# Kernel tuning notes

Measured on AMD Instinct MI355X. Metric: run time of the kernel, lower is better.

## Reference

```python
import jax, jax.numpy as jnp
import numpy as np

N = 50000
D = 64
E = 800000


def setup_inputs() -> dict:
    key = jax.random.key(0)
    ks = jax.random.split(key, 8)
    x = jax.random.normal(ks[0], (N, D), dtype=jnp.float32)
    edge_index = jax.random.randint(ks[1], (2, E), 0, N, dtype=jnp.int64)
    edge_attr = jax.random.normal(ks[2], (E,), dtype=jnp.float32)
    x_agg_emb = jax.random.normal(ks[3], (N, D), dtype=jnp.float32)
    # Linear(2D -> D) weights stored as [in, out]; scale ~ kaiming-ish
    W_msg = jax.random.normal(ks[4], (2 * D, D), dtype=jnp.float32) * (1.0 / np.sqrt(2 * D))
    b_msg = jnp.zeros((D,), dtype=jnp.float32)
    W_upd = jax.random.normal(ks[5], (2 * D, D), dtype=jnp.float32) * (1.0 / np.sqrt(2 * D))
    b_upd = jnp.zeros((D,), dtype=jnp.float32)
    return {"x": x, "edge_index": edge_index, "edge_attr": edge_attr,
            "x_agg_emb": x_agg_emb, "W_msg": W_msg, "b_msg": b_msg,
            "W_upd": W_upd, "b_upd": b_upd}


def reference(x, edge_index, edge_attr, x_agg_emb, W_msg, b_msg, W_upd, b_upd):
    col, row = edge_index[0], edge_index[1]
    # edge-weighted gather: [E, D]
    msgs = edge_attr[:, None] * x[col]
    # scatter-mean over destination nodes (dim_size = N)
    summed = jax.ops.segment_sum(msgs, row, num_segments=N)            # [N, D]
    counts = jax.ops.segment_sum(jnp.ones_like(edge_attr), row, num_segments=N)  # [N]
    x_agg = summed / jnp.maximum(counts, 1.0)[:, None]
    # message MLP: Linear(2D->D) + ReLU
    m = jax.nn.relu(jnp.concatenate([x_agg, x_agg_emb], axis=-1) @ W_msg + b_msg)
    # update MLP: Linear(2D->D) + ReLU
    out = jax.nn.relu(jnp.concatenate([x, m], axis=-1) @ W_upd + b_upd)
    return out
```

## Files before the change

### kernel.cpp

```cpp
#include <hip/hip_runtime.h>


#define CAP 48
#define FILLB 2048
#define CVTB 1024

typedef __attribute__((ext_vector_type(8))) short short8;
typedef __attribute__((ext_vector_type(4))) float f32x4;

__device__ __forceinline__ unsigned short f2bf(float f) {
    unsigned int u = __float_as_uint(f);
    u += 0x7FFFu + ((u >> 16) & 1u);
    return (unsigned short)(u >> 16);
}
__device__ __forceinline__ float bf2f(unsigned short h) {
    return __uint_as_float((unsigned)h << 16);
}
__device__ __forceinline__ uint4 pack8(const float* v) {
    uint4 r;
    r.x = (unsigned)f2bf(v[0]) | ((unsigned)f2bf(v[1]) << 16);
    r.y = (unsigned)f2bf(v[2]) | ((unsigned)f2bf(v[3]) << 16);
    r.z = (unsigned)f2bf(v[4]) | ((unsigned)f2bf(v[5]) << 16);
    r.w = (unsigned)f2bf(v[6]) | ((unsigned)f2bf(v[7]) << 16);
    return r;
}

__global__ __launch_bounds__(256) void zero_f32(float* p, int n) {
    int i = blockIdx.x * 256 + threadIdx.x;
    if (i < n) p[i] = 0.0f;
}
__global__ __launch_bounds__(256) void zero_i32(int* p, int n) {
    int i = blockIdx.x * 256 + threadIdx.x;
    if (i < n) p[i] = 0;
}

__global__ __launch_bounds__(256) void cvt_zero_group(
    const float* __restrict__ x, unsigned short* __restrict__ xh,
    int* __restrict__ cnt, uint4* __restrict__ pk4, int N)
{
    const int g    = blockIdx.x & 7;
    const int bg   = blockIdx.x >> 3;
    const int nb   = gridDim.x >> 3;
    const int rpg  = (N + 7) >> 3;
    const int rlo  = g * rpg;
    const int rhi  = min(rlo + rpg, N);
    const int nrows = rhi - rlo;
    const int tid  = bg * 256 + (int)threadIdx.x;
    const int nthr = nb * 256;

    for (int c = tid; c < nrows * 8; c += nthr) {
        size_t base = ((size_t)rlo * 8 + c) * 8;
        const float* src = x + base;
        float4 p0 = ((const float4*)src)[0];
        float4 p1 = ((const float4*)src)[1];
        float v[8];
        v[0] = p0.x; v[1] = p0.y; v[2] = p0.z; v[3] = p0.w;
        v[4] = p1.x; v[5] = p1.y; v[6] = p1.z; v[7] = p1.w;
        *(uint4*)&xh[base] = pack8(v);
    }
    for (int c = tid; c < nrows; c += nthr) cnt[rlo + c] = 0;
    const uint4 z = make_uint4(0u, 0u, 0u, 0u);
    const size_t pbase = (size_t)rlo * (CAP / 2);
    for (size_t c = tid; c < (size_t)nrows * (CAP / 2); c += nthr)
        pk4[pbase + c] = z;
}

__global__ __launch_bounds__(256) void fill_group_kernel(
    const int* __restrict__ ei, const float* __restrict__ ea,
    int* cnt, int2* __restrict__ packed, int E, int N)
{
    const int g   = blockIdx.x & 7;
    const int bg  = blockIdx.x >> 3;
    const int nb  = gridDim.x >> 3;
    const int rpg = (N + 7) >> 3;
    const int rlo = g * rpg;
    const int rhi = min(rlo + rpg, N);
    const int chunk = (E + nb - 1) / nb;
    const int lo = bg * chunk;
    const int hi = min(lo + chunk, E);
    int e = lo + (int)threadIdx.x;
    for (; e + 768 < hi; e += 1024) {
        int r0 = ei[E + e];
        int r1 = ei[E + e + 256];
        int r2 = ei[E + e + 512];
        int r3 = ei[E + e + 768];
        int c0 = ei[e], c1 = ei[e + 256], c2 = ei[e + 512], c3 = ei[e + 768];
        float a0 = ea[e], a1 = ea[e + 256], a2 = ea[e + 512], a3 = ea[e + 768];
        bool m0 = (r0 >= rlo) & (r0 < rhi);
        bool m1 = (r1 >= rlo) & (r1 < rhi);
        bool m2 = (r2 >= rlo) & (r2 < rhi);
        bool m3 = (r3 >= rlo) & (r3 < rhi);
        int p0 = CAP, p1 = CAP, p2 = CAP, p3 = CAP;
        if (m0) p0 = atomicAdd(&cnt[r0], 1);
        if (m1) p1 = atomicAdd(&cnt[r1], 1);
        if (m2) p2 = atomicAdd(&cnt[r2], 1);
        if (m3) p3 = atomicAdd(&cnt[r3], 1);
        if (m0 && p0 < CAP) packed[(size_t)r0 * CAP + p0] = make_int2(c0, __float_as_int(a0));
        if (m1 && p1 < CAP) packed[(size_t)r1 * CAP + p1] = make_int2(c1, __float_as_int(a1));
        if (m2 && p2 < CAP) packed[(size_t)r2 * CAP + p2] = make_int2(c2, __float_as_int(a2));
        if (m3 && p3 < CAP) packed[(size_t)r3 * CAP + p3] = make_int2(c3, __float_as_int(a3));
    }
    for (; e < hi; e += 256) {
        int row = ei[E + e];
        if (row >= rlo && row < rhi) {
            int pos = atomicAdd(&cnt[row], 1);
            if (pos < CAP)
                packed[(size_t)row * CAP + pos] = make_int2(ei[e], __float_as_int(ea[e]));
        }
    }
}


__device__ __forceinline__ void stage_W512(
    unsigned short* Wb, const float* Wg, int t)
{
    #pragma unroll
    for (int c = t; c < 1024; c += 512) {
        int R = c >> 6, nn = c & 63;
        int kt = R >> 2, qq = R & 3;
        const float* src = Wg + (size_t)(kt * 32 + qq * 8) * 64 + nn;
        float v[8];
        #pragma unroll
        for (int j = 0; j < 8; j++) v[j] = src[(size_t)j * 64];
        *(uint4*)&Wb[R * 528 + nn * 8] = pack8(v);
    }
}

__global__ __launch_bounds__(512, 6) void gather_mlp(
    const int2* __restrict__ packed, const int* __restrict__ cnt,
    const unsigned short* __restrict__ xh, const float* __restrict__ emb,
    const float* __restrict__ Wm, const float* __restrict__ bm,
    const float* __restrict__ Wu, const float* __restrict__ bu,
    float* __restrict__ out, int N)
{
    __shared__ __align__(16) unsigned short Ab [64 * 128];
    __shared__ __align__(16) unsigned short Wb [16 * 528];
    __shared__ __align__(16) unsigned short Wb2[16 * 528];

    const int t    = threadIdx.x;
    const int g    = blockIdx.x & 7;
    const int tile = blockIdx.x >> 3;
    const int rpg  = (N + 7) >> 3;
    const int rlo  = g * rpg;
    const int rhi  = min(rlo + rpg, N);
    const int tile0 = rlo + tile * 64;
    const int lane = t & 63;
    const int q = lane >> 4, ln = lane & 15;
    const unsigned lane2 = (unsigned)lane * 2;
    const int wu = __builtin_amdgcn_readfirstlane(t >> 6);

    stage_W512(Wb,  Wm, t);
    stage_W512(Wb2, Wu, t);
    const int sr = t >> 3, sc = t & 7;
    uint4 xreg = make_uint4(0u, 0u, 0u, 0u);
    if (tile0 + sr < rhi)
        xreg = *(const uint4*)&xh[(size_t)(tile0 + sr) * 64 + sc * 8];
    {
        int node = tile0 + sr;
        float v[8] = {0.f, 0.f, 0.f, 0.f, 0.f, 0.f, 0.f, 0.f};
        if (node < rhi) {
            const float* src = emb + (size_t)node * 64 + sc * 8;
            float4 p0 = ((const float4*)src)[0];
            float4 p1 = ((const float4*)src)[1];
            v[0] = p0.x; v[1] = p0.y; v[2] = p0.z; v[3] = p0.w;
            v[4] = p1.x; v[5] = p1.y; v[6] = p1.z; v[7] = p1.w;
        }
        int ch = 8 + sc;
        *(uint4*)&Ab[sr * 128 + ((ch ^ (sr & 15)) * 8)] = pack8(v);
    }

    const int4* sp[8];
    int deg[8];
    int maxdl = 0;
    #pragma unroll
    for (int n = 0; n < 8; n++) {
        int node = tile0 + wu * 8 + n;
        bool ok = node < rhi;
        int nd = ok ? node : rlo;
        sp[n] = (const int4*)packed + (size_t)nd * (CAP / 2);
        deg[n] = ok ? __builtin_amdgcn_readfirstlane(cnt[node]) : 0;
        maxdl = max(maxdl, min(deg[n], CAP));
    }
    float ac0[8], ac1[8];
    #pragma unroll
    for (int n = 0; n < 8; n++) { ac0[n] = 0.f; ac1[n] = 0.f; }

    const int maxb = (maxdl + 1) >> 1;
    for (int jb = 0; jb < maxb; jb++) {
        {
            int4 d0 = sp[0][jb], d1 = sp[1][jb], d2 = sp[2][jb], d3 = sp[3][jb];
            unsigned short u00 = *(const unsigned short*)((const char*)xh + (((unsigned)d0.x << 7) + lane2));
            unsigned short u01 = *(const unsigned short*)((const char*)xh + (((unsigned)d0.z << 7) + lane2));
            unsigned short u10 = *(const unsigned short*)((const char*)xh + (((unsigned)d1.x << 7) + lane2));
            unsigned short u11 = *(const unsigned short*)((const char*)xh + (((unsigned)d1.z << 7) + lane2));
            unsigned short u20 = *(const unsigned short*)((const char*)xh + (((unsigned)d2.x << 7) + lane2));
            unsigned short u21 = *(const unsigned short*)((const char*)xh + (((unsigned)d2.z << 7) + lane2));
            unsigned short u30 = *(const unsigned short*)((const char*)xh + (((unsigned)d3.x << 7) + lane2));
            unsigned short u31 = *(const unsigned short*)((const char*)xh + (((unsigned)d3.z << 7) + lane2));
            ac0[0] += __int_as_float(d0.y) * bf2f(u00);
            ac1[0] += __int_as_float(d0.w) * bf2f(u01);
            ac0[1] += __int_as_float(d1.y) * bf2f(u10);
            ac1[1] += __int_as_float(d1.w) * bf2f(u11);
            ac0[2] += __int_as_float(d2.y) * bf2f(u20);
            ac1[2] += __int_as_float(d2.w) * bf2f(u21);
            ac0[3] += __int_as_float(d3.y) * bf2f(u30);
            ac1[3] += __int_as_float(d3.w) * bf2f(u31);
        }
        {
            int4 d0 = sp[4][jb], d1 = sp[5][jb], d2 = sp[6][jb], d3 = sp[7][jb];
            unsigned short u00 = *(const unsigned short*)((const char*)xh + (((unsigned)d0.x << 7) + lane2));
            unsigned short u01 = *(const unsigned short*)((const char*)xh + (((unsigned)d0.z << 7) + lane2));
            unsigned short u10 = *(const unsigned short*)((const char*)xh + (((unsigned)d1.x << 7) + lane2));
            unsigned short u11 = *(const unsigned short*)((const char*)xh + (((unsigned)d1.z << 7) + lane2));
            unsigned short u20 = *(const unsigned short*)((const char*)xh + (((unsigned)d2.x << 7) + lane2));
            unsigned short u21 = *(const unsigned short*)((const char*)xh + (((unsigned)d2.z << 7) + lane2));
            unsigned short u30 = *(const unsigned short*)((const char*)xh + (((unsigned)d3.x << 7) + lane2));
            unsigned short u31 = *(const unsigned short*)((const char*)xh + (((unsigned)d3.z << 7) + lane2));
            ac0[4] += __int_as_float(d0.y) * bf2f(u00);
            ac1[4] += __int_as_float(d0.w) * bf2f(u01);
            ac0[5] += __int_as_float(d1.y) * bf2f(u10);
            ac1[5] += __int_as_float(d1.w) * bf2f(u11);
            ac0[6] += __int_as_float(d2.y) * bf2f(u20);
            ac1[6] += __int_as_float(d2.w) * bf2f(u21);
            ac0[7] += __int_as_float(d3.y) * bf2f(u30);
            ac1[7] += __int_as_float(d3.w) * bf2f(u31);
        }
    }

    #pragma unroll
    for (int n = 0; n < 8; n++) {
        int r = wu * 8 + n;
        int node = tile0 + r;
        float mean = (node < rhi)
            ? (ac0[n] + ac1[n]) / fmaxf((float)deg[n], 1.0f) : 0.f;
        int ch = lane >> 3;
        Ab[r * 128 + ((ch ^ (r & 15)) * 8) + (lane & 7)] = f2bf(mean);
    }
    __syncthreads();

    const int wr = wu & 3;
    const int wn0 = (wu >> 2) * 2, wn1 = wn0 + 1;
    f32x4 acc0 = (f32x4){0.f, 0.f, 0.f, 0.f};
    f32x4 acc1 = (f32x4){0.f, 0.f, 0.f, 0.f};
    {
        const int rr = wr * 16 + ln;
        #pragma unroll
        for (int kt = 0; kt < 4; kt++) {
            short8 af = *(const short8*)&Ab[rr * 128 + (((kt * 4 + q) ^ ln) * 8)];
            short8 bf0 = *(const short8*)&Wb[(kt * 4 + q) * 528 + (wn0 * 16 + ln) * 8];
            short8 bf1 = *(const short8*)&Wb[(kt * 4 + q) * 528 + (wn1 * 16 + ln) * 8];
            acc0 = __builtin_amdgcn_mfma_f32_16x16x32_bf16(af, bf0, acc0, 0, 0, 0);
            acc1 = __builtin_amdgcn_mfma_f32_16x16x32_bf16(af, bf1, acc1, 0, 0, 0);
        }
    }
    __syncthreads();

    *(uint4*)&Ab[sr * 128 + ((sc ^ (sr & 15)) * 8)] = xreg;
    {
        float bmv0 = bm[wn0 * 16 + ln];
        float bmv1 = bm[wn1 * 16 + ln];
        #pragma unroll
        for (int reg = 0; reg < 4; reg++) {
            int rr = wr * 16 + q * 4 + reg;
            {
                float mv = fmaxf(acc0[reg] + bmv0, 0.f);
                int k  = 64 + wn0 * 16 + ln;
                int ch = k >> 3;
                Ab[rr * 128 + ((ch ^ (rr & 15)) * 8) + (k & 7)] = f2bf(mv);
            }
            {
                float mv = fmaxf(acc1[reg] + bmv1, 0.f);
                int k  = 64 + wn1 * 16 + ln;
                int ch = k >> 3;
                Ab[rr * 128 + ((ch ^ (rr & 15)) * 8) + (k & 7)] = f2bf(mv);
            }
        }
    }
    __syncthreads();

    f32x4 acc2a = (f32x4){0.f, 0.f, 0.f, 0.f};
    f32x4 acc2b = (f32x4){0.f, 0.f, 0.f, 0.f};
    {
        const int rr = wr * 16 + ln;
        #pragma unroll
        for (int kt = 0; kt < 4; kt++) {
            short8 af = *(const short8*)&Ab[rr * 128 + (((kt * 4 + q) ^ ln) * 8)];
            short8 bf0 = *(const short8*)&Wb2[(kt * 4 + q) * 528 + (wn0 * 16 + ln) * 8];
            short8 bf1 = *(const short8*)&Wb2[(kt * 4 + q) * 528 + (wn1 * 16 + ln) * 8];
            acc2a = __builtin_amdgcn_mfma_f32_16x16x32_bf16(af, bf0, acc2a, 0, 0, 0);
            acc2b = __builtin_amdgcn_mfma_f32_16x16x32_bf16(af, bf1, acc2b, 0, 0, 0);
        }
    }
    {
        float buv0 = bu[wn0 * 16 + ln];
        float buv1 = bu[wn1 * 16 + ln];
        #pragma unroll
        for (int reg = 0; reg < 4; reg++) {
            int rr = wr * 16 + q * 4 + reg;
            int node = tile0 + rr;
            if (node < rhi) {
                out[(size_t)node * 64 + wn0 * 16 + ln] = fmaxf(acc2a[reg] + buv0, 0.f);
                out[(size_t)node * 64 + wn1 * 16 + ln] = fmaxf(acc2b[reg] + buv1, 0.f);
            }
        }
    }
}


__global__ __launch_bounds__(256) void hist_kernel(
    const int* __restrict__ ei, int* hist, int E)
{
    int e = blockIdx.x * 256 + threadIdx.x;
    if (e < E) atomicAdd(&hist[ei[E + e]], 1);
}
__global__ __launch_bounds__(256) void scan_partial_kernel(
    const int* __restrict__ hist, int* partial, int N)
{
    __shared__ int s[256];
    int t = threadIdx.x;
    int i = blockIdx.x * 256 + t;
    s[t] = (i < N) ? hist[i] : 0;
    __syncthreads();
    #pragma unroll
    for (int off = 128; off > 0; off >>= 1) {
        if (t < off) s[t] += s[t + off];
        __syncthreads();
    }
    if (t == 0) partial[blockIdx.x] = s[0];
}
__global__ __launch_bounds__(256) void scan_top_kernel(
    const int* __restrict__ partial, int* scanP, int NB)
{
    __shared__ int s[256];
    int t = threadIdx.x;
    int v = (t < NB) ? partial[t] : 0;
    s[t] = v;
    __syncthreads();
    #pragma unroll
    for (int off = 1; off < 256; off <<= 1) {
        int add = (t >= off) ? s[t - off] : 0;
        __syncthreads();
        s[t] += add;
        __syncthreads();
    }
    if (t < NB) scanP[t] = s[t] - v;
}
__global__ __launch_bounds__(256) void scan_final_kernel(
    const int* __restrict__ hist, const int* __restrict__ scanP,
    int* offsets, int* cursor, int N)
{
    __shared__ int s[256];
    int t = threadIdx.x;
    int i = blockIdx.x * 256 + t;
    int v = (i < N) ? hist[i] : 0;
    s[t] = v;
    __syncthreads();
    #pragma unroll
    for (int off = 1; off < 256; off <<= 1) {
        int add = (t >= off) ? s[t - off] : 0;
        __syncthreads();
        s[t] += add;
        __syncthreads();
    }
    if (i < N) {
        int o = scanP[blockIdx.x] + s[t] - v;
        offsets[i] = o;
        cursor[i]  = o;
    }
}
__global__ __launch_bounds__(256) void fill_kernel(
    const int* __restrict__ ei, const float* __restrict__ ea,
    int* cursor, int2* __restrict__ packed, int E)
{
    int e = blockIdx.x * 256 + threadIdx.x;
    if (e >= E) return;
    int pos = atomicAdd(&cursor[ei[E + e]], 1);
    packed[pos] = make_int2(ei[e], __float_as_int(ea[e]));
}
__global__ __launch_bounds__(256) void gather_kernel(
    const int2* __restrict__ packed, const int* __restrict__ offsets,
    const int* __restrict__ hist, const float* __restrict__ x,
    float* __restrict__ out, int N)
{
    int t = threadIdx.x;
    int n = blockIdx.x * 4 + (t >> 6);
    int lane = t & 63;
    if (n >= N) return;
    int start = offsets[n];
    int deg   = hist[n];
    float a0 = 0.f, a1 = 0.f, a2 = 0.f, a3 = 0.f;
    int j = 0;
    for (; j + 4 <= deg; j += 4) {
        int2 p0 = packed[start + j];
        int2 p1 = packed[start + j + 1];
        int2 p2 = packed[start + j + 2];
        int2 p3 = packed[start + j + 3];
        a0 += __int_as_float(p0.y) * x[(size_t)p0.x * 64 + lane];
        a1 += __int_as_float(p1.y) * x[(size_t)p1.x * 64 + lane];
        a2 += __int_as_float(p2.y) * x[(size_t)p2.x * 64 + lane];
        a3 += __int_as_float(p3.y) * x[(size_t)p3.x * 64 + lane];
    }
    for (; j < deg; j++) {
        int2 p = packed[start + j];
        a0 += __int_as_float(p.y) * x[(size_t)p.x * 64 + lane];
    }
    float acc = (a0 + a1) + (a2 + a3);
    out[(size_t)n * 64 + lane] = acc / fmaxf((float)deg, 1.0f);
}


__global__ __launch_bounds__(256) void scatter_kernel(
    const int* __restrict__ ei, const float* __restrict__ ea,
    const float* __restrict__ x, float* summed, float* counts, int E)
{
    int idx = blockIdx.x * 256 + threadIdx.x;
    int e = idx >> 6;
    int d = idx & 63;
    if (e >= E) return;
    float v = ea[e] * x[(size_t)ei[e] * 64 + d];
    atomicAdd(&summed[(size_t)ei[E + e] * 64 + d], v);
    if (d == 0) atomicAdd(&counts[ei[E + e]], 1.0f);
}


__device__ __forceinline__ void stage_W(
    unsigned short* Wb, const float* Wg, int t)
{
    #pragma unroll
    for (int c = t; c < 1024; c += 256) {
        int R = c >> 6, nn = c & 63;
        int kt = R >> 2, qq = R & 3;
        const float* src = Wg + (size_t)(kt * 32 + qq * 8) * 64 + nn;
        float v[8];
        #pragma unroll
        for (int j = 0; j < 8; j++) v[j] = src[(size_t)j * 64];
        *(uint4*)&Wb[R * 528 + nn * 8] = pack8(v);
    }
}

__device__ __forceinline__ void mfma_tile(
    const unsigned short* Ab, const unsigned short* Wb,
    int wv, int lane, f32x4 acc[4])
{
    const int q  = lane >> 4;
    const int ln = lane & 15;
    const int rr = wv * 16 + ln;
    short8 af[4];
    #pragma unroll
    for (int kt = 0; kt < 4; kt++)
        af[kt] = *(const short8*)&Ab[rr * 128 + (((kt * 4 + q) ^ ln) * 8)];
    #pragma unroll
    for (int nt = 0; nt < 4; nt++) {
        #pragma unroll
        for (int kt = 0; kt < 4; kt++) {
            short8 bf = *(const short8*)&Wb[(kt * 4 + q) * 528 + (nt * 16 + ln) * 8];
            acc[nt] = __builtin_amdgcn_mfma_f32_16x16x32_bf16(af[kt], bf, acc[nt], 0, 0, 0);
        }
    }
}

__global__ __launch_bounds__(256) void mfma_mlp(
    const float* Aagg, const float* __restrict__ Aemb,
    const float* __restrict__ counts, const float* __restrict__ Xin,
    const float* __restrict__ Wm, const float* __restrict__ bm,
    const float* __restrict__ Wu, const float* __restrict__ bu,
    float* out, int N)
{
    __shared__ __align__(16) unsigned short Ab[64 * 128];
    __shared__ __align__(16) unsigned short Wb[16 * 528];

    const int t = threadIdx.x;
    const int tile0 = blockIdx.x * 64;
    const int lane = t & 63, wv = t >> 6;
    const int q = lane >> 4, ln = lane & 15;

    stage_W(Wb, Wm, t);
    #pragma unroll
    for (int s = t; s < 1024; s += 256) {
        int r = s >> 4, chunk = s & 15;
        int node = tile0 + r;
        float v[8] = {0.f, 0.f, 0.f, 0.f, 0.f, 0.f, 0.f, 0.f};
        if (node < N) {
            const float* src = (chunk < 8)
                ? (Aagg + (size_t)node * 64 + chunk * 8)
                : (Aemb + (size_t)node * 64 + (chunk - 8) * 8);
            float4 p0 = ((const float4*)src)[0];
            float4 p1 = ((const float4*)src)[1];
            v[0] = p0.x; v[1] = p0.y; v[2] = p0.z; v[3] = p0.w;
            v[4] = p1.x; v[5] = p1.y; v[6] = p1.z; v[7] = p1.w;
            if (counts && chunk < 8) {
                float rc = 1.0f / fmaxf(counts[node], 1.0f);
                #pragma unroll
                for (int i = 0; i < 8; i++) v[i] *= rc;
            }
        }
        *(uint4*)&Ab[r * 128 + ((chunk ^ (r & 15)) * 8)] = pack8(v);
    }
    __syncthreads();

    f32x4 acc[4];
    #pragma unroll
    for (int nt = 0; nt < 4; nt++) acc[nt] = (f32x4){0.f, 0.f, 0.f, 0.f};
    mfma_tile(Ab, Wb, wv, lane, acc);
    __syncthreads();

    stage_W(Wb, Wu, t);
    #pragma unroll
    for (int s = t; s < 512; s += 256) {
        int r = s >> 3, chunk = s & 7;
        int node = tile0 + r;
        float v[8] = {0.f, 0.f, 0.f, 0.f, 0.f, 0.f, 0.f, 0.f};
        if (node < N) {
            const float* src = Xin + (size_t)node * 64 + chunk * 8;
            float4 p0 = ((const float4*)src)[0];
            float4 p1 = ((const float4*)src)[1];
            v[0] = p0.x; v[1] = p0.y; v[2] = p0.z; v[3] = p0.w;
            v[4] = p1.x; v[5] = p1.y; v[6] = p1.z; v[7] = p1.w;
        }
        *(uint4*)&Ab[r * 128 + ((chunk ^ (r & 15)) * 8)] = pack8(v);
    }
    #pragma unroll
    for (int nt = 0; nt < 4; nt++) {
        float bmv = bm[nt * 16 + ln];
        #pragma unroll
        for (int reg = 0; reg < 4; reg++) {
            float mv = fmaxf(acc[nt][reg] + bmv, 0.f);
            int rr = wv * 16 + q * 4 + reg;
            int k  = 64 + nt * 16 + ln;
            int ch = k >> 3;
            Ab[rr * 128 + ((ch ^ (rr & 15)) * 8) + (k & 7)] = f2bf(mv);
        }
    }
    __syncthreads();

    f32x4 acc2[4];
    #pragma unroll
    for (int nt = 0; nt < 4; nt++) acc2[nt] = (f32x4){0.f, 0.f, 0.f, 0.f};
    mfma_tile(Ab, Wb, wv, lane, acc2);
    #pragma unroll
    for (int nt = 0; nt < 4; nt++) {
        float buv = bu[nt * 16 + ln];
        #pragma unroll
        for (int reg = 0; reg < 4; reg++) {
            int rr = wv * 16 + q * 4 + reg;
            int node = tile0 + rr;
            if (node < N)
                out[(size_t)node * 64 + nt * 16 + ln] =
                    fmaxf(acc2[nt][reg] + buv, 0.f);
        }
    }
}

extern "C" void kernel_launch(void* const* d_in, const int* in_sizes, int n_in,
                              void* d_out, int out_size, void* d_ws, size_t ws_size,
                              hipStream_t stream) {
    const float* x   = (const float*)d_in[0];
    const int*   ei  = (const int*)d_in[1];
    const float* ea  = (const float*)d_in[2];
    const float* emb = (const float*)d_in[3];
    const float* Wm  = (const float*)d_in[4];
    const float* bm  = (const float*)d_in[5];
    const float* Wu  = (const float*)d_in[6];
    const float* bu  = (const float*)d_in[7];
    float*       out = (float*)d_out;

    const int N = in_sizes[0] / 64;
    const int E = in_sizes[2];
    const int NB = (N + 255) / 256;

    const int eblocks = (E + 255) / 256;
    const int mblocks = (N + 63) / 64;
    const int rpg = (N + 7) / 8;

    const size_t need_cap = (size_t)N * CAP * 8 + (size_t)N * 128 + (size_t)N * 4;
    const size_t need_csr = (size_t)E * 8 + ((size_t)3 * N + 512) * 4;

    if (ws_size >= need_cap) {
        char* ws = (char*)d_ws;
        int2*           packed = (int2*)ws;
        unsigned short* xh     = (unsigned short*)(ws + (size_t)N * CAP * 8);
        int*            cnt    = (int*)(ws + (size_t)N * CAP * 8 + (size_t)N * 128);

        cvt_zero_group<<<CVTB, 256, 0, stream>>>(x, xh, cnt, (uint4*)packed, N);
        fill_group_kernel<<<FILLB, 256, 0, stream>>>(ei, ea, cnt, packed, E, N);
        int tpg = (rpg + 63) / 64;
        gather_mlp<<<8 * tpg, 512, 0, stream>>>(packed, cnt, xh, emb,
                                                Wm, bm, Wu, bu, out, N);
    } else if (ws_size >= need_csr && NB <= 256) {
        char* ws = (char*)d_ws;
        int2* packed  = (int2*)ws;
        int*  hist    = (int*)(ws + (size_t)E * 8);
        int*  offsets = hist + N;
        int*  cursor  = offsets + N;
        int*  partial = cursor + N;
        int*  scanP   = partial + 256;

        zero_i32<<<NB, 256, 0, stream>>>(hist, N);
        hist_kernel<<<eblocks, 256, 0, stream>>>(ei, hist, E);
        scan_partial_kernel<<<NB, 256, 0, stream>>>(hist, partial, N);
        scan_top_kernel<<<1, 256, 0, stream>>>(partial, scanP, NB);
        scan_final_kernel<<<NB, 256, 0, stream>>>(hist, scanP, offsets, cursor, N);
        fill_kernel<<<eblocks, 256, 0, stream>>>(ei, ea, cursor, packed, E);
        gather_kernel<<<(N + 3) / 4, 256, 0, stream>>>(packed, offsets, hist, x, out, N);
        mfma_mlp<<<mblocks, 256, 0, stream>>>(out, emb, nullptr, x,
                                              Wm, bm, Wu, bu, out, N);
    } else {
        float* counts = (float*)d_ws;
        zero_f32<<<(N * 64 + 255) / 256, 256, 0, stream>>>(out, N * 64);
        zero_f32<<<NB, 256, 0, stream>>>(counts, N);
        long long total = (long long)E * 64;
        scatter_kernel<<<(int)((total + 255) / 256), 256, 0, stream>>>(
            ei, ea, x, out, counts, E);
        mfma_mlp<<<mblocks, 256, 0, stream>>>(out, emb, counts, x,
                                              Wm, bm, Wu, bu, out, N);
    }
}
```

Measured before the change: 163.8 us.

## Fuse convert, fill and gather-MLP into one cooperative kernel with grid syncs

Replaces the three-kernel sequence (convert/zero, bucketed fill, gather+MLP) with a single cooperative kernel of 512 blocks that separates the phases with grid-wide syncs and loops over tiles persistently. The aim is to remove the launch gaps and tail effects between kernels. The cost is two grid barriers, a fixed grid size that may underfill or overfill the device, and a lower occupancy hint. The fallback gather_mlp also drops readfirstlane on the degrees and loses its occupancy hint.

After: 506.5 us. +209.1%, slower.

```diff
diff --git a/kernel.cpp b/kernel.cpp
--- a/kernel.cpp
+++ b/kernel.cpp
@@ -1,7 +1,11 @@
 #include <hip/hip_runtime.h>
+#include <hip/hip_cooperative_groups.h>
+
+namespace cg = cooperative_groups;
 
 
 #define CAP 48
+#define FGRID 512
 #define FILLB 2048
 #define CVTB 1024
 
@@ -33,6 +37,275 @@
     int i = blockIdx.x * 256 + threadIdx.x;
     if (i < n) p[i] = 0;
 }
+
+__device__ __forceinline__ void stage_W512(
+    unsigned short* Wb, const float* Wg, int t)
+{
+    #pragma unroll
+    for (int c = t; c < 1024; c += 512) {
+        int R = c >> 6, nn = c & 63;
+        int kt = R >> 2, qq = R & 3;
+        const float* src = Wg + (size_t)(kt * 32 + qq * 8) * 64 + nn;
+        float v[8];
+        #pragma unroll
+        for (int j = 0; j < 8; j++) v[j] = src[(size_t)j * 64];
+        *(uint4*)&Wb[R * 528 + nn * 8] = pack8(v);
+    }
+}
+
+__global__ __launch_bounds__(512, 4) void fused_all(
+    const float* __restrict__ x, const int* __restrict__ ei,
+    const float* __restrict__ ea, const float* __restrict__ emb,
+    const float* __restrict__ Wm, const float* __restrict__ bm,
+    const float* __restrict__ Wu, const float* __restrict__ bu,
+    float* __restrict__ out, int2* __restrict__ packed,
+    unsigned short* __restrict__ xh, int* __restrict__ cnt,
+    int N, int E)
+{
+    __shared__ __align__(16) unsigned short Ab [64 * 128];
+    __shared__ __align__(16) unsigned short Wb [16 * 528];
+    __shared__ __align__(16) unsigned short Wb2[16 * 528];
+
+    cg::grid_group grid = cg::this_grid();
+
+    const int t   = threadIdx.x;
+    const int g   = blockIdx.x & 7;
+    const int bg  = blockIdx.x >> 3;
+    const int nb  = gridDim.x >> 3;
+    const int rpg = (N + 7) >> 3;
+    const int rlo = g * rpg;
+    const int rhi = min(rlo + rpg, N);
+    const int nrows = rhi - rlo;
+
+    {
+        const int tid  = bg * 512 + t;
+        const int nthr = nb * 512;
+        for (int c = tid; c < nrows * 8; c += nthr) {
+            size_t base = ((size_t)rlo * 8 + c) * 8;
+            const float* src = x + base;
+            float4 p0 = ((const float4*)src)[0];
+            float4 p1 = ((const float4*)src)[1];
+            float v[8];
+            v[0] = p0.x; v[1] = p0.y; v[2] = p0.z; v[3] = p0.w;
+            v[4] = p1.x; v[5] = p1.y; v[6] = p1.z; v[7] = p1.w;
+            *(uint4*)&xh[base] = pack8(v);
+        }
+        for (int c = tid; c < nrows; c += nthr) cnt[rlo + c] = 0;
+        const uint4 z = make_uint4(0u, 0u, 0u, 0u);
+        uint4* pk4 = (uint4*)packed;
+        const size_t pbase = (size_t)rlo * (CAP / 2);
+        for (int c = tid; c < nrows * (CAP / 2); c += nthr)
+            pk4[pbase + c] = z;
+    }
+    __threadfence();
+    grid.sync();
+
+    {
+        const int chunk = (E + nb - 1) / nb;
+        const int lo = bg * chunk;
+        const int hi = min(lo + chunk, E);
+        int e = lo + t;
+        for (; e + 1536 < hi; e += 2048) {
+            int r0 = ei[E + e], r1 = ei[E + e + 512];
+            int r2 = ei[E + e + 1024], r3 = ei[E + e + 1536];
+            int c0 = ei[e], c1 = ei[e + 512], c2 = ei[e + 1024], c3 = ei[e + 1536];
+            float a0 = ea[e], a1 = ea[e + 512], a2 = ea[e + 1024], a3 = ea[e + 1536];
+            bool m0 = (r0 >= rlo) & (r0 < rhi);
+            bool m1 = (r1 >= rlo) & (r1 < rhi);
+            bool m2 = (r2 >= rlo) & (r2 < rhi);
+            bool m3 = (r3 >= rlo) & (r3 < rhi);
+            int p0 = CAP, p1 = CAP, p2 = CAP, p3 = CAP;
+            if (m0) p0 = atomicAdd(&cnt[r0], 1);
+            if (m1) p1 = atomicAdd(&cnt[r1], 1);
+            if (m2) p2 = atomicAdd(&cnt[r2], 1);
+            if (m3) p3 = atomicAdd(&cnt[r3], 1);
+            if (m0 && p0 < CAP) packed[(size_t)r0 * CAP + p0] = make_int2(c0, __float_as_int(a0));
+            if (m1 && p1 < CAP) packed[(size_t)r1 * CAP + p1] = make_int2(c1, __float_as_int(a1));
+            if (m2 && p2 < CAP) packed[(size_t)r2 * CAP + p2] = make_int2(c2, __float_as_int(a2));
+            if (m3 && p3 < CAP) packed[(size_t)r3 * CAP + p3] = make_int2(c3, __float_as_int(a3));
+        }
+        for (; e < hi; e += 512) {
+            int row = ei[E + e];
+            if (row >= rlo && row < rhi) {
+                int pos = atomicAdd(&cnt[row], 1);
+                if (pos < CAP)
+                    packed[(size_t)row * CAP + pos] = make_int2(ei[e], __float_as_int(ea[e]));
+            }
+        }
+    }
+    __threadfence();
+    grid.sync();
+
+    stage_W512(Wb,  Wm, t);
+    stage_W512(Wb2, Wu, t);
+
+    const int lane = t & 63;
+    const int q = lane >> 4, ln = lane & 15;
+    const unsigned lane2 = (unsigned)lane * 2;
+    const int wu = __builtin_amdgcn_readfirstlane(t >> 6);
+    const int wr = wu & 3;
+    const int wn0 = (wu >> 2) * 2, wn1 = wn0 + 1;
+    const int sr = t >> 3, sc = t & 7;
+    const int TPG = (rpg + 63) >> 6;
+
+    for (int tile = bg; tile < TPG; tile += nb) {
+        const int tile0 = rlo + tile * 64;
+
+        uint4 xreg = make_uint4(0u, 0u, 0u, 0u);
+        if (tile0 + sr < rhi)
+            xreg = *(const uint4*)&xh[(size_t)(tile0 + sr) * 64 + sc * 8];
+        {
+            int node = tile0 + sr;
+            float v[8] = {0.f, 0.f, 0.f, 0.f, 0.f, 0.f, 0.f, 0.f};
+            if (node < rhi) {
+                const float* src = emb + (size_t)node * 64 + sc * 8;
+                float4 p0 = ((const float4*)src)[0];
+                float4 p1 = ((const float4*)src)[1];
+                v[0] = p0.x; v[1] = p0.y; v[2] = p0.z; v[3] = p0.w;
+                v[4] = p1.x; v[5] = p1.y; v[6] = p1.z; v[7] = p1.w;
+            }
+            int ch = 8 + sc;
+            *(uint4*)&Ab[sr * 128 + ((ch ^ (sr & 15)) * 8)] = pack8(v);
+        }
+
+        int seg[8], deg[8];
+        int maxdl = 0;
+        #pragma unroll
+        for (int n = 0; n < 8; n++) {
+            int node = tile0 + wu * 8 + n;
+            bool ok = node < rhi;
+            seg[n] = (ok ? node : rlo) * (CAP / 2);
+            deg[n] = ok ? cnt[node] : 0;
+            maxdl = max(maxdl, min(deg[n], CAP));
+        }
+        float ac0[8], ac1[8];
+        #pragma unroll
+        for (int n = 0; n < 8; n++) { ac0[n] = 0.f; ac1[n] = 0.f; }
+
+        const int4* s4 = (const int4*)packed;
+        const int maxb = (maxdl + 1) >> 1;
+        for (int jb = 0; jb < maxb; jb++) {
+            {
+                int4 d0 = s4[seg[0] + jb], d1 = s4[seg[1] + jb];
+                int4 d2 = s4[seg[2] + jb], d3 = s4[seg[3] + jb];
+                unsigned short u00 = *(const unsigned short*)((const char*)xh + (((unsigned)d0.x << 7) + lane2));
+                unsigned short u01 = *(const unsigned short*)((const char*)xh + (((unsigned)d0.z << 7) + lane2));
+                unsigned short u10 = *(const unsigned short*)((const char*)xh + (((unsigned)d1.x << 7) + lane2));
+                unsigned short u11 = *(const unsigned short*)((const char*)xh + (((unsigned)d1.z << 7) + lane2));
+                unsigned short u20 = *(const unsigned short*)((const char*)xh + (((unsigned)d2.x << 7) + lane2));
+                unsigned short u21 = *(const unsigned short*)((const char*)xh + (((unsigned)d2.z << 7) + lane2));
+                unsigned short u30 = *(const unsigned short*)((const char*)xh + (((unsigned)d3.x << 7) + lane2));
+                unsigned short u31 = *(const unsigned short*)((const char*)xh + (((unsigned)d3.z << 7) + lane2));
+                ac0[0] += __int_as_float(d0.y) * bf2f(u00);
+                ac1[0] += __int_as_float(d0.w) * bf2f(u01);
+                ac0[1] += __int_as_float(d1.y) * bf2f(u10);
+                ac1[1] += __int_as_float(d1.w) * bf2f(u11);
+                ac0[2] += __int_as_float(d2.y) * bf2f(u20);
+                ac1[2] += __int_as_float(d2.w) * bf2f(u21);
+                ac0[3] += __int_as_float(d3.y) * bf2f(u30);
+                ac1[3] += __int_as_float(d3.w) * bf2f(u31);
+            }
+            {
+                int4 d0 = s4[seg[4] + jb], d1 = s4[seg[5] + jb];
+                int4 d2 = s4[seg[6] + jb], d3 = s4[seg[7] + jb];
+                unsigned short u00 = *(const unsigned short*)((const char*)xh + (((unsigned)d0.x << 7) + lane2));
+                unsigned short u01 = *(const unsigned short*)((const char*)xh + (((unsigned)d0.z << 7) + lane2));
+                unsigned short u10 = *(const unsigned short*)((const char*)xh + (((unsigned)d1.x << 7) + lane2));
+                unsigned short u11 = *(const unsigned short*)((const char*)xh + (((unsigned)d1.z << 7) + lane2));
+                unsigned short u20 = *(const unsigned short*)((const char*)xh + (((unsigned)d2.x << 7) + lane2));
+                unsigned short u21 = *(const unsigned short*)((const char*)xh + (((unsigned)d2.z << 7) + lane2));
+                unsigned short u30 = *(const unsigned short*)((const char*)xh + (((unsigned)d3.x << 7) + lane2));
+                unsigned short u31 = *(const unsigned short*)((const char*)xh + (((unsigned)d3.z << 7) + lane2));
+                ac0[4] += __int_as_float(d0.y) * bf2f(u00);
+                ac1[4] += __int_as_float(d0.w) * bf2f(u01);
+                ac0[5] += __int_as_float(d1.y) * bf2f(u10);
+                ac1[5] += __int_as_float(d1.w) * bf2f(u11);
+                ac0[6] += __int_as_float(d2.y) * bf2f(u20);
+                ac1[6] += __int_as_float(d2.w) * bf2f(u21);
+                ac0[7] += __int_as_float(d3.y) * bf2f(u30);
+                ac1[7] += __int_as_float(d3.w) * bf2f(u31);
+            }
+        }
+
+        #pragma unroll
+        for (int n = 0; n < 8; n++) {
+            int r = wu * 8 + n;
+            int node = tile0 + r;
+            float mean = (node < rhi)
+                ? (ac0[n] + ac1[n]) / fmaxf((float)deg[n], 1.0f) : 0.f;
+            int ch = lane >> 3;
+            Ab[r * 128 + ((ch ^ (r & 15)) * 8) + (lane & 7)] = f2bf(mean);
+        }
+        __syncthreads();
+
+        f32x4 acc0 = (f32x4){0.f, 0.f, 0.f, 0.f};
+        f32x4 acc1 = (f32x4){0.f, 0.f, 0.f, 0.f};
+        {
+            const int rr = wr * 16 + ln;
+            #pragma unroll
+            for (int kt = 0; kt < 4; kt++) {
+                short8 af  = *(const short8*)&Ab[rr * 128 + (((kt * 4 + q) ^ ln) * 8)];
+                short8 bf0 = *(const short8*)&Wb[(kt * 4 + q) * 528 + (wn0 * 16 + ln) * 8];
+                short8 bf1 = *(const short8*)&Wb[(kt * 4 + q) * 528 + (wn1 * 16 + ln) * 8];
+                acc0 = __builtin_amdgcn_mfma_f32_16x16x32_bf16(af, bf0, acc0, 0, 0, 0);
+                acc1 = __builtin_amdgcn_mfma_f32_16x16x32_bf16(af, bf1, acc1, 0, 0, 0);
+            }
+        }
+        __syncthreads();
+
+        *(uint4*)&Ab[sr * 128 + ((sc ^ (sr & 15)) * 8)] = xreg;
+        {
+            float bmv0 = bm[wn0 * 16 + ln];
+            float bmv1 = bm[wn1 * 16 + ln];
+            #pragma unroll
+            for (int reg = 0; reg < 4; reg++) {
+                int rr = wr * 16 + q * 4 + reg;
+                {
+                    float mv = fmaxf(acc0[reg] + bmv0, 0.f);
+                    int k  = 64 + wn0 * 16 + ln;
+                    int ch = k >> 3;
+                    Ab[rr * 128 + ((ch ^ (rr & 15)) * 8) + (k & 7)] = f2bf(mv);
+                }
+                {
+                    float mv = fmaxf(acc1[reg] + bmv1, 0.f);
+                    int k  = 64 + wn1 * 16 + ln;
+                    int ch = k >> 3;
+                    Ab[rr * 128 + ((ch ^ (rr & 15)) * 8) + (k & 7)] = f2bf(mv);
+                }
+            }
+        }
+        __syncthreads();
+
+        f32x4 acc2a = (f32x4){0.f, 0.f, 0.f, 0.f};
+        f32x4 acc2b = (f32x4){0.f, 0.f, 0.f, 0.f};
+        {
+            const int rr = wr * 16 + ln;
+            #pragma unroll
+            for (int kt = 0; kt < 4; kt++) {
+                short8 af  = *(const short8*)&Ab[rr * 128 + (((kt * 4 + q) ^ ln) * 8)];
+                short8 bf0 = *(const short8*)&Wb2[(kt * 4 + q) * 528 + (wn0 * 16 + ln) * 8];
+                short8 bf1 = *(const short8*)&Wb2[(kt * 4 + q) * 528 + (wn1 * 16 + ln) * 8];
+                acc2a = __builtin_amdgcn_mfma_f32_16x16x32_bf16(af, bf0, acc2a, 0, 0, 0);
+                acc2b = __builtin_amdgcn_mfma_f32_16x16x32_bf16(af, bf1, acc2b, 0, 0, 0);
+            }
+        }
+        {
+            float buv0 = bu[wn0 * 16 + ln];
+            float buv1 = bu[wn1 * 16 + ln];
+            #pragma unroll
+            for (int reg = 0; reg < 4; reg++) {
+                int rr = wr * 16 + q * 4 + reg;
+                int node = tile0 + rr;
+                if (node < rhi) {
+                    out[(size_t)node * 64 + wn0 * 16 + ln] = fmaxf(acc2a[reg] + buv0, 0.f);
+                    out[(size_t)node * 64 + wn1 * 16 + ln] = fmaxf(acc2b[reg] + buv1, 0.f);
+                }
+            }
+        }
+        __syncthreads();
+    }
+}
+
 
 __global__ __launch_bounds__(256) void cvt_zero_group(
     const float* __restrict__ x, unsigned short* __restrict__ xh,
@@ -110,23 +383,7 @@
     }
 }
 
-
-__device__ __forceinline__ void stage_W512(
-    unsigned short* Wb, const float* Wg, int t)
-{
-    #pragma unroll
-    for (int c = t; c < 1024; c += 512) {
-        int R = c >> 6, nn = c & 63;
-        int kt = R >> 2, qq = R & 3;
-        const float* src = Wg + (size_t)(kt * 32 + qq * 8) * 64 + nn;
-        float v[8];
-        #pragma unroll
-        for (int j = 0; j < 8; j++) v[j] = src[(size_t)j * 64];
-        *(uint4*)&Wb[R * 528 + nn * 8] = pack8(v);
-    }
-}
-
-__global__ __launch_bounds__(512, 6) void gather_mlp(
+__global__ __launch_bounds__(512) void gather_mlp(
     const int2* __restrict__ packed, const int* __restrict__ cnt,
     const unsigned short* __restrict__ xh, const float* __restrict__ emb,
     const float* __restrict__ Wm, const float* __restrict__ bm,
@@ -169,26 +426,28 @@
         *(uint4*)&Ab[sr * 128 + ((ch ^ (sr & 15)) * 8)] = pack8(v);
     }
 
-    const int4* sp[8];
-    int deg[8];
+    int seg[8], deg[8];
     int maxdl = 0;
     #pragma unroll
     for (int n = 0; n < 8; n++) {
         int node = tile0 + wu * 8 + n;
         bool ok = node < rhi;
-        int nd = ok ? node : rlo;
-        sp[n] = (const int4*)packed + (size_t)nd * (CAP / 2);
-        deg[n] = ok ? __builtin_amdgcn_readfirstlane(cnt[node]) : 0;
+        seg[n] = (ok ? node : rlo) * (CAP / 2);
+        deg[n] = ok ? cnt[node] : 0;
         maxdl = max(maxdl, min(deg[n], CAP));
     }
     float ac0[8], ac1[8];
     #pragma unroll
     for (int n = 0; n < 8; n++) { ac0[n] = 0.f; ac1[n] = 0.f; }
 
+    const int4* s4 = (const int4*)packed;
     const int maxb = (maxdl + 1) >> 1;
     for (int jb = 0; jb < maxb; jb++) {
-        {
-            int4 d0 = sp[0][jb], d1 = sp[1][jb], d2 = sp[2][jb], d3 = sp[3][jb];
+        #pragma unroll
+        for (int h = 0; h < 2; h++) {
+            int b = h * 4;
+            int4 d0 = s4[seg[b] + jb], d1 = s4[seg[b + 1] + jb];
+            int4 d2 = s4[seg[b + 2] + jb], d3 = s4[seg[b + 3] + jb];
             unsigned short u00 = *(const unsigned short*)((const char*)xh + (((unsigned)d0.x << 7) + lane2));
             unsigned short u01 = *(const unsigned short*)((const char*)xh + (((unsigned)d0.z << 7) + lane2));
             unsigned short u10 = *(const unsigned short*)((const char*)xh + (((unsigned)d1.x << 7) + lane2));
@@ -197,33 +456,14 @@
             unsigned short u21 = *(const unsigned short*)((const char*)xh + (((unsigned)d2.z << 7) + lane2));
             unsigned short u30 = *(const unsigned short*)((const char*)xh + (((unsigned)d3.x << 7) + lane2));
             unsigned short u31 = *(const unsigned short*)((const char*)xh + (((unsigned)d3.z << 7) + lane2));
-            ac0[0] += __int_as_float(d0.y) * bf2f(u00);
-            ac1[0] += __int_as_float(d0.w) * bf2f(u01);
-            ac0[1] += __int_as_float(d1.y) * bf2f(u10);
-            ac1[1] += __int_as_float(d1.w) * bf2f(u11);
-            ac0[2] += __int_as_float(d2.y) * bf2f(u20);
-            ac1[2] += __int_as_float(d2.w) * bf2f(u21);
-            ac0[3] += __int_as_float(d3.y) * bf2f(u30);
-            ac1[3] += __int_as_float(d3.w) * bf2f(u31);
-        }
-        {
-            int4 d0 = sp[4][jb], d1 = sp[5][jb], d2 = sp[6][jb], d3 = sp[7][jb];
-            unsigned short u00 = *(const unsigned short*)((const char*)xh + (((unsigned)d0.x << 7) + lane2));
-            unsigned short u01 = *(const unsigned short*)((const char*)xh + (((unsigned)d0.z << 7) + lane2));
-            unsigned short u10 = *(const unsigned short*)((const char*)xh + (((unsigned)d1.x << 7) + lane2));
-            unsigned short u11 = *(const unsigned short*)((const char*)xh + (((unsigned)d1.z << 7) + lane2));
-            unsigned short u20 = *(const unsigned short*)((const char*)xh + (((unsigned)d2.x << 7) + lane2));
-            unsigned short u21 = *(const unsigned short*)((const char*)xh + (((unsigned)d2.z << 7) + lane2));
-            unsigned short u30 = *(const unsigned short*)((const char*)xh + (((unsigned)d3.x << 7) + lane2));
-            unsigned short u31 = *(const unsigned short*)((const char*)xh + (((unsigned)d3.z << 7) + lane2));
-            ac0[4] += __int_as_float(d0.y) * bf2f(u00);
-            ac1[4] += __int_as_float(d0.w) * bf2f(u01);
-            ac0[5] += __int_as_float(d1.y) * bf2f(u10);
-            ac1[5] += __int_as_float(d1.w) * bf2f(u11);
-            ac0[6] += __int_as_float(d2.y) * bf2f(u20);
-            ac1[6] += __int_as_float(d2.w) * bf2f(u21);
-            ac0[7] += __int_as_float(d3.y) * bf2f(u30);
-            ac1[7] += __int_as_float(d3.w) * bf2f(u31);
+            ac0[b]     += __int_as_float(d0.y) * bf2f(u00);
+            ac1[b]     += __int_as_float(d0.w) * bf2f(u01);
+            ac0[b + 1] += __int_as_float(d1.y) * bf2f(u10);
+            ac1[b + 1] += __int_as_float(d1.w) * bf2f(u11);
+            ac0[b + 2] += __int_as_float(d2.y) * bf2f(u20);
+            ac1[b + 2] += __int_as_float(d2.w) * bf2f(u21);
+            ac0[b + 3] += __int_as_float(d3.y) * bf2f(u30);
+            ac1[b + 3] += __int_as_float(d3.w) * bf2f(u31);
         }
     }
 
@@ -246,7 +486,7 @@
         const int rr = wr * 16 + ln;
         #pragma unroll
         for (int kt = 0; kt < 4; kt++) {
-            short8 af = *(const short8*)&Ab[rr * 128 + (((kt * 4 + q) ^ ln) * 8)];
+            short8 af  = *(const short8*)&Ab[rr * 128 + (((kt * 4 + q) ^ ln) * 8)];
             short8 bf0 = *(const short8*)&Wb[(kt * 4 + q) * 528 + (wn0 * 16 + ln) * 8];
             short8 bf1 = *(const short8*)&Wb[(kt * 4 + q) * 528 + (wn1 * 16 + ln) * 8];
             acc0 = __builtin_amdgcn_mfma_f32_16x16x32_bf16(af, bf0, acc0, 0, 0, 0);
@@ -284,7 +524,7 @@
         const int rr = wr * 16 + ln;
         #pragma unroll
         for (int kt = 0; kt < 4; kt++) {
-            short8 af = *(const short8*)&Ab[rr * 128 + (((kt * 4 + q) ^ ln) * 8)];
+            short8 af  = *(const short8*)&Ab[rr * 128 + (((kt * 4 + q) ^ ln) * 8)];
             short8 bf0 = *(const short8*)&Wb2[(kt * 4 + q) * 528 + (wn0 * 16 + ln) * 8];
             short8 bf1 = *(const short8*)&Wb2[(kt * 4 + q) * 528 + (wn1 * 16 + ln) * 8];
             acc2a = __builtin_amdgcn_mfma_f32_16x16x32_bf16(af, bf0, acc2a, 0, 0, 0);
@@ -408,7 +648,6 @@
     out[(size_t)n * 64 + lane] = acc / fmaxf((float)deg, 1.0f);
 }
 
-
 __global__ __launch_bounds__(256) void scatter_kernel(
     const int* __restrict__ ei, const float* __restrict__ ea,
     const float* __restrict__ x, float* summed, float* counts, int E)
@@ -564,8 +803,8 @@
     const float* bu  = (const float*)d_in[7];
     float*       out = (float*)d_out;
 
-    const int N = in_sizes[0] / 64;
-    const int E = in_sizes[2];
+    int N = in_sizes[0] / 64;
+    int E = in_sizes[2];
     const int NB = (N + 255) / 256;
 
     const int eblocks = (E + 255) / 256;
@@ -581,11 +820,22 @@
         unsigned short* xh     = (unsigned short*)(ws + (size_t)N * CAP * 8);
         int*            cnt    = (int*)(ws + (size_t)N * CAP * 8 + (size_t)N * 128);
 
-        cvt_zero_group<<<CVTB, 256, 0, stream>>>(x, xh, cnt, (uint4*)packed, N);
-        fill_group_kernel<<<FILLB, 256, 0, stream>>>(ei, ea, cnt, packed, E, N);
-        int tpg = (rpg + 63) / 64;
-        gather_mlp<<<8 * tpg, 512, 0, stream>>>(packed, cnt, xh, emb,
-                                                Wm, bm, Wu, bu, out, N);
+        void* kargs[] = {
+            (void*)&x, (void*)&ei, (void*)&ea, (void*)&emb,
+            (void*)&Wm, (void*)&bm, (void*)&Wu, (void*)&bu,
+            (void*)&out, (void*)&packed, (void*)&xh, (void*)&cnt,
+            (void*)&N, (void*)&E
+        };
+        hipError_t ce = hipLaunchCooperativeKernel(
+            reinterpret_cast<void*>(fused_all), dim3(FGRID), dim3(512),
+            kargs, 0, stream);
+        if (ce != hipSuccess) {
+            cvt_zero_group<<<CVTB, 256, 0, stream>>>(x, xh, cnt, (uint4*)packed, N);
+            fill_group_kernel<<<FILLB, 256, 0, stream>>>(ei, ea, cnt, packed, E, N);
+            int tpg = (rpg + 63) / 64;
+            gather_mlp<<<8 * tpg, 512, 0, stream>>>(packed, cnt, xh, emb,
+                                                    Wm, bm, Wu, bu, out, N);
+        }
     } else if (ws_size >= need_csr && NB <= 256) {
         char* ws = (char*)d_ws;
         int2* packed  = (int2*)ws;
```
